# Optimization experiments

Measured on AMD Instinct MI355X. Metric: run time of the kernel, lower is better.

Reference implementation:

```python
import jax, jax.numpy as jnp
import numpy as np

N_HEADS = 8
FACTOR = 5


def layer_norm(x, g, b, eps=1e-5):
    m = x.mean(-1, keepdims=True)
    v = ((x - m) ** 2).mean(-1, keepdims=True)
    return (x - m) / jnp.sqrt(v + eps) * g + b


def prob_attn(q, k, v, factor, key):
    # q,k,v: [B,H,L,E]; mask_flag=False path of ProbAttention
    B, H, L, E = q.shape
    U = min(int(factor * np.ceil(np.log(L))), L)  # sample_k == n_top (L_Q == L_K)
    idx = jax.random.randint(key, (L, U), 0, L)   # random KV sample per query pos
    k_samp = k[:, :, idx, :]                      # gather: [B,H,L,U,E]
    qk_samp = jnp.einsum('bhle,bhlue->bhlu', q, k_samp)
    M = qk_samp.max(-1) - qk_samp.sum(-1) / L     # sparsity measure [B,H,L]
    _, top = jax.lax.top_k(M, U)                  # top-u query indices [B,H,U]
    q_red = jnp.take_along_axis(q, top[..., None], axis=2)  # [B,H,U,E]
    scores = jnp.einsum('bhue,bhke->bhuk', q_red, k) * (1.0 / np.sqrt(E))
    attn = jax.nn.softmax(scores, axis=-1)
    upd = jnp.einsum('bhuk,bhkd->bhud', attn, v)  # [B,H,U,D]
    ctx = jnp.broadcast_to(v.mean(axis=2, keepdims=True), (B, H, L, v.shape[-1]))
    bi = jnp.arange(B)[:, None, None]
    hi = jnp.arange(H)[None, :, None]
    return ctx.at[bi, hi, top].set(upd)          # scatter reduced context


def informer_fwd(x_enc, x_mark_enc, conv_w, Wq, bq, Wk, bk, Wv, bv, Wo, bo,
                 W1, b1, W2, b2, g1, be1, g2, be2, gF, bF, fc_w, fc_b):
    B, L, C = x_enc.shape
    D = conv_w.shape[0]
    H = N_HEADS
    dh = D // H
    # TokenEmbedding: circular Conv1d k=3, no bias
    xp = jnp.transpose(x_enc, (0, 2, 1))                      # [B,C,L]
    xp = jnp.concatenate([xp[..., -1:], xp, xp[..., :1]], axis=-1)
    tok = jax.lax.conv_general_dilated(xp, conv_w, (1,), 'VALID',
                                       dimension_numbers=('NCH', 'OIH', 'NCH'))
    tok = jnp.transpose(tok, (0, 2, 1))                       # [B,L,D]
    # PositionalEmbedding (sinusoid)
    pos = jnp.arange(L, dtype=jnp.float32)[:, None]
    div = jnp.exp(jnp.arange(0, D, 2, dtype=jnp.float32) * (-np.log(10000.0) / D))
    pe = jnp.zeros((L, D), jnp.float32)
    pe = pe.at[:, 0::2].set(jnp.sin(pos * div)).at[:, 1::2].set(jnp.cos(pos * div))
    x = tok + pe
    n_layers = Wq.shape[0]
    for l in range(n_layers):
        q = (x @ Wq[l].T + bq[l]).reshape(B, L, H, dh).transpose(0, 2, 1, 3)
        k = (x @ Wk[l].T + bk[l]).reshape(B, L, H, dh).transpose(0, 2, 1, 3)
        v = (x @ Wv[l].T + bv[l]).reshape(B, L, H, dh).transpose(0, 2, 1, 3)
        ctx = prob_attn(q, k, v, FACTOR, jax.random.fold_in(jax.random.key(42), l))
        # NOTE: original code does .view(B, L, -1) on [B,H,L,dh] WITHOUT transposing
        out = ctx.reshape(B, L, H * dh)
        x = x + (out @ Wo[l].T + bo[l])
        x = layer_norm(x, g1[l], be1[l])
        y = jax.nn.relu(x @ W1[l].T + b1[l]) @ W2[l].T + b2[l]   # 1x1 convs == dense
        x = layer_norm(x + y, g2[l], be2[l])
    x = layer_norm(x, gF, bF)
    out = x * x_mark_enc[..., None]
    out = out.reshape(B, -1)
    return out @ fc_w.T + fc_b


def setup_inputs() -> dict:
    B, L, C, D, H, Dff, EL, NC = 8, 1024, 32, 512, 8, 2048, 3, 16
    key = jax.random.key(0)
    ks = jax.random.split(key, 16)
    rn = lambda k, s, sc=0.02: sc * jax.random.normal(k, s, dtype=jnp.float32)
    return {
        'x_enc': jax.random.normal(ks[0], (B, L, C), dtype=jnp.float32),
        'x_mark_enc': jax.random.uniform(ks[1], (B, L), dtype=jnp.float32),
        'conv_w': rn(ks[2], (D, C, 3), 0.1),
        'Wq': rn(ks[3], (EL, D, D)), 'bq': jnp.zeros((EL, D)),
        'Wk': rn(ks[4], (EL, D, D)), 'bk': jnp.zeros((EL, D)),
        'Wv': rn(ks[5], (EL, D, D)), 'bv': jnp.zeros((EL, D)),
        'Wo': rn(ks[6], (EL, D, D)), 'bo': jnp.zeros((EL, D)),
        'W1': rn(ks[7], (EL, Dff, D)), 'b1': jnp.zeros((EL, Dff)),
        'W2': rn(ks[8], (EL, D, Dff)), 'b2': jnp.zeros((EL, D)),
        'g1': jnp.ones((EL, D)), 'be1': jnp.zeros((EL, D)),
        'g2': jnp.ones((EL, D)), 'be2': jnp.zeros((EL, D)),
        'gF': jnp.ones((D,)), 'bF': jnp.zeros((D,)),
        'fc_w': rn(ks[9], (NC, L * D)), 'fc_b': jnp.zeros((NC,)),
    }


def reference(x_enc, x_mark_enc, conv_w, Wq, bq, Wk, bk, Wv, bv, Wo, bo,
              W1, b1, W2, b2, g1, be1, g2, be2, gF, bF, fc_w, fc_b):
    return informer_fwd(x_enc, x_mark_enc, conv_w, Wq, bq, Wk, bk, Wv, bv, Wo, bo,
                        W1, b1, W2, b2, g1, be1, g2, be2, gF, bF, fc_w, fc_b)
```

## Files before the change

kernel.cpp:

```cpp
#include <hip/hip_runtime.h>
#include <stdint.h>
#include <math.h>

#define LSEQ   1024
#define DMODEL 512
#define NH     8
#define DH     64
#define DFF    2048
#define NB     8
#define NLAYER 3
#define UTOP   35
#define NCLS   16
#define WPERL  3145728

typedef unsigned short u16;
typedef _Float16 f16x8 __attribute__((ext_vector_type(8)));
typedef __attribute__((ext_vector_type(4))) float f32x4;

__device__ __forceinline__ u16 f2h(float f) {
  _Float16 h = (_Float16)f;
  return __builtin_bit_cast(u16, h);
}
__device__ __forceinline__ float h2f(u16 b) {
  return (float)__builtin_bit_cast(_Float16, b);
}

#define GLDS16(gsrc, ldst)                                                        \
  __builtin_amdgcn_global_load_lds(                                              \
      (const __attribute__((address_space(1))) void*)(gsrc),                     \
      (__attribute__((address_space(3))) void*)(ldst), 16, 0, 0)

__host__ __device__ __forceinline__ uint32_t rotl32(uint32_t x, int d) {
  return (x << d) | (x >> (32 - d));
}
__host__ __device__ inline void tf2x32(uint32_t k0, uint32_t k1,
                                       uint32_t c0, uint32_t c1,
                                       uint32_t& o0, uint32_t& o1) {
  uint32_t ks2 = k0 ^ k1 ^ 0x1BD11BDAu;
  uint32_t x0 = c0 + k0, x1 = c1 + k1;
#define TF_R4(a,b,c,d) \
  x0 += x1; x1 = rotl32(x1,(a)); x1 ^= x0; \
  x0 += x1; x1 = rotl32(x1,(b)); x1 ^= x0; \
  x0 += x1; x1 = rotl32(x1,(c)); x1 ^= x0; \
  x0 += x1; x1 = rotl32(x1,(d)); x1 ^= x0;
  TF_R4(13,15,26,6)   x0 += k1;  x1 += ks2 + 1u;
  TF_R4(17,29,16,24)  x0 += ks2; x1 += k0 + 2u;
  TF_R4(13,15,26,6)   x0 += k0;  x1 += k1 + 3u;
  TF_R4(17,29,16,24)  x0 += k1;  x1 += ks2 + 4u;
  TF_R4(13,15,26,6)   x0 += ks2; x1 += k0 + 5u;
#undef TF_R4
  o0 = x0; o1 = x1;
}

__global__ void __launch_bounds__(256) gen_idx_kernel(uint32_t k0, uint32_t k1,
                                                      int* idx) {
  int i = blockIdx.x * 256 + threadIdx.x;
  if (i >= LSEQ * UTOP) return;
  uint32_t a, b;
  tf2x32(k0, k1, 0u, (uint32_t)i, a, b);
  idx[i] = (int)((a ^ b) & (LSEQ - 1));
}

__global__ void __launch_bounds__(256) cvt_all(
    const float* __restrict__ Wq, const float* __restrict__ Wk,
    const float* __restrict__ Wv, const float* __restrict__ Wo,
    const float* __restrict__ W1, const float* __restrict__ W2,
    u16* __restrict__ dst) {
  const size_t total = (size_t)NLAYER * WPERL;
  for (size_t i4 = ((size_t)blockIdx.x * 256 + threadIdx.x) * 4;
       i4 < total; i4 += (size_t)gridDim.x * 256 * 4) {
    int l = (int)(i4 / WPERL);
    int off = (int)(i4 % WPERL);
    const float* src; size_t so;
    if (off < 262144)       { src = Wq; so = (size_t)l * 262144  + off; }
    else if (off < 524288)  { src = Wk; so = (size_t)l * 262144  + off - 262144; }
    else if (off < 786432)  { src = Wv; so = (size_t)l * 262144  + off - 524288; }
    else if (off < 1048576) { src = Wo; so = (size_t)l * 262144  + off - 786432; }
    else if (off < 2097152) { src = W1; so = (size_t)l * 1048576 + off - 1048576; }
    else                    { src = W2; so = (size_t)l * 1048576 + off - 2097152; }
    float4 v = *(const float4*)&src[so];
    ushort4 h;
    h.x = f2h(v.x); h.y = f2h(v.y); h.z = f2h(v.z); h.w = f2h(v.w);
    *(ushort4*)&dst[i4] = h;
  }
}

__global__ void __launch_bounds__(256) conv_pe(const float* __restrict__ xe,
                                               const float* __restrict__ w,
                                               float* __restrict__ xout,
                                               u16* __restrict__ xh) {
  const int d0 = blockIdx.x * 64;
  const int l0 = blockIdx.y * 32;
  const int b  = blockIdx.z;
  const int tid = threadIdx.x;
  const int dl = tid & 63;
  const int lq = tid >> 6;
  __shared__ float ws_[64][97];
  __shared__ float xs[32][37];

  for (int i = tid; i < 64 * 96; i += 256) {
    int dd = i / 96, cc = i - dd * 96;
    ws_[dd][cc] = w[(size_t)(d0 + dd) * 96 + cc];
  }
  for (int i = tid; i < 34 * 32; i += 256) {
    int r = i >> 5, c = i & 31;
    int row = (l0 - 1 + r + LSEQ) & (LSEQ - 1);
    xs[c][r] = xe[((size_t)b * LSEQ + row) * 32 + c];
  }

  const int d = d0 + dl;
  float div = expf((float)(d & ~1) * (-9.210340371976184f / 512.0f));
  float pe[8];
  #pragma unroll
  for (int j = 0; j < 8; ++j) {
    float arg = (float)(l0 + lq * 8 + j) * div;
    pe[j] = (d & 1) ? cosf(arg) : sinf(arg);
  }
  __syncthreads();

  float acc[8] = {};
  #pragma unroll 4
  for (int c = 0; c < 32; ++c) {
    float w0 = ws_[dl][c * 3 + 0];
    float w1 = ws_[dl][c * 3 + 1];
    float w2 = ws_[dl][c * 3 + 2];
    float xv[10];
    #pragma unroll
    for (int r = 0; r < 10; ++r) xv[r] = xs[c][lq * 8 + r];
    #pragma unroll
    for (int j = 0; j < 8; ++j)
      acc[j] += xv[j] * w0 + xv[j + 1] * w1 + xv[j + 2] * w2;
  }
  #pragma unroll
  for (int j = 0; j < 8; ++j) {
    int l = l0 + lq * 8 + j;
    float v = acc[j] + pe[j];
    size_t m = (size_t)b * LSEQ + l;
    xout[m * DMODEL + d] = v;
    xh[m * DMODEL + d] = f2h(v);
  }
}

__global__ void __launch_bounds__(512, 2) gemm256(
    const u16* __restrict__ A, const u16* __restrict__ W,
    const float* __restrict__ bias, const float* __restrict__ bias_k,
    const float* __restrict__ bias_v,
    float* __restrict__ Cf, u16* __restrict__ C2,
    int Kseg, int N, int mode) {
  __shared__ u16 As[2][256 * 64];
  __shared__ u16 Bs[2][256 * 64];
  const int tid = threadIdx.x;
  const int lane = tid & 63, wv = tid >> 6;
  const int wm = wv >> 2, wn = wv & 3;
  const int pid = blockIdx.y * gridDim.x + blockIdx.x;
  const int cpx = (gridDim.x * gridDim.y) >> 3;
  const int swz = (pid & 7) * cpx + (pid >> 3);
  const int m0 = (swz / gridDim.x) * 256, n0 = (swz % gridDim.x) * 256;
  const int lrow = lane >> 3;
  const int kgS = (lane & 7) ^ lrow;
  const int nt = Kseg >> 6;

  f32x4 acc[8][4];
  #pragma unroll
  for (int i = 0; i < 8; ++i)
    #pragma unroll
    for (int j = 0; j < 4; ++j) acc[i][j] = (f32x4){0.f, 0.f, 0.f, 0.f};

  auto STAGE = [&](int kv, int buf) {
    #pragma unroll
    for (int r = 0; r < 4; ++r) {
      int seg = wv * 4 + r;
      int row = seg * 8 + lrow;
      GLDS16(A + (size_t)(m0 + row) * Kseg + kv + kgS * 8, &As[buf][seg * 512]);
      GLDS16(W + (size_t)(n0 + row) * Kseg + kv + kgS * 8, &Bs[buf][seg * 512]);
    }
  };

  STAGE(0, 0);
  for (int t = 0; t < nt; ++t) {
    const int cur = t & 1;
    if (t + 1 < nt) {
      STAGE((t + 1) * 64, cur ^ 1);
      asm volatile("s_waitcnt vmcnt(8)" ::: "memory");
    } else {
      asm volatile("s_waitcnt vmcnt(0)" ::: "memory");
    }
    __builtin_amdgcn_s_barrier();
    __builtin_amdgcn_sched_barrier(0);
    #pragma unroll
    for (int kk = 0; kk < 2; ++kk) {
      int kg = kk * 4 + (lane >> 4);
      f16x8 af[8], bf[4];
      #pragma unroll
      for (int mi = 0; mi < 8; ++mi) {
        int row = wm * 128 + mi * 16 + (lane & 15);
        af[mi] = *(const f16x8*)&As[cur][row * 64 + ((kg ^ (row & 7)) << 3)];
      }
      #pragma unroll
      for (int ni = 0; ni < 4; ++ni) {
        int row = wn * 64 + ni * 16 + (lane & 15);
        bf[ni] = *(const f16x8*)&Bs[cur][row * 64 + ((kg ^ (row & 7)) << 3)];
      }
      #pragma unroll
      for (int mi = 0; mi < 8; ++mi)
        #pragma unroll
        for (int ni = 0; ni < 4; ++ni)
          acc[mi][ni] = __builtin_amdgcn_mfma_f32_16x16x32_f16(
              af[mi], bf[ni], acc[mi][ni], 0, 0, 0);
    }
    __builtin_amdgcn_s_barrier();
  }

  const int colb = n0 + wn * 64 + (lane & 15);
  const int rowb = m0 + wm * 128 + ((lane >> 4) << 2);
  #pragma unroll
  for (int mi = 0; mi < 8; ++mi) {
    #pragma unroll
    for (int ni = 0; ni < 4; ++ni) {
      int gcol = colb + ni * 16;
      float bv;
      if (mode == 3) {
        int mat = gcol >> 9, c = gcol & 511;
        bv = (mat == 0 ? bias : (mat == 1 ? bias_k : bias_v))[c];
      } else {
        bv = bias[gcol];
      }
      #pragma unroll
      for (int j = 0; j < 4; ++j) {
        int grow = rowb + mi * 16 + j;
        float v = acc[mi][ni][j] + bv;
        if (mode == 1) {
          C2[(size_t)grow * N + gcol] = f2h(fmaxf(v, 0.f));
        } else {
          int mat = gcol >> 9, c = gcol & 511;
          Cf[(size_t)mat * (NB * LSEQ * DMODEL) +
             (size_t)(grow >> 10) * (NH * LSEQ * DH) +
             (size_t)(c >> 6) * (LSEQ * DH) +
             (size_t)(grow & (LSEQ - 1)) * DH + (c & (DH - 1))] = v;
        }
      }
    }
  }
}

__global__ void __launch_bounds__(256) gemm_cat(
    const u16* __restrict__ A, const u16* __restrict__ W,
    const float* __restrict__ bias, const float* __restrict__ resid,
    float* __restrict__ Cf, float* __restrict__ Cf1,
    int Kseg, int kslice, int N) {
  __shared__ u16 As[2][128 * 64];
  __shared__ u16 Bs[2][128 * 64];
  const int tid = threadIdx.x;
  const int lane = tid & 63, wv = tid >> 6;
  const int wm = wv >> 1, wn = wv & 1;
  const int pid = blockIdx.y * gridDim.x + blockIdx.x;
  const int cpx = (gridDim.x * gridDim.y) >> 3;
  const int swz = (pid & 7) * cpx + (pid >> 3);
  const int m0 = (swz / gridDim.x) * 128, n0 = (swz % gridDim.x) * 128;
  const int lrow = lane >> 3;
  const int kgS = (lane & 7) ^ lrow;
  const int kv0 = blockIdx.z * kslice;
  const int nt = kslice >> 6;

  f32x4 acc[4][4];
  #pragma unroll
  for (int i = 0; i < 4; ++i)
    #pragma unroll
    for (int j = 0; j < 4; ++j) acc[i][j] = (f32x4){0.f, 0.f, 0.f, 0.f};

  auto STAGE = [&](int kv, int buf) {
    #pragma unroll
    for (int r = 0; r < 4; ++r) {
      int seg = wv * 4 + r;
      int row = seg * 8 + lrow;
      GLDS16(A + (size_t)(m0 + row) * Kseg + kv + kgS * 8, &As[buf][seg * 512]);
      GLDS16(W + (size_t)(n0 + row) * Kseg + kv + kgS * 8, &Bs[buf][seg * 512]);
    }
  };

  STAGE(kv0, 0);
  for (int t = 0; t < nt; ++t) {
    const int cur = t & 1;
    if (t + 1 < nt) {
      STAGE(kv0 + (t + 1) * 64, cur ^ 1);
      asm volatile("s_waitcnt vmcnt(8)" ::: "memory");
    } else {
      asm volatile("s_waitcnt vmcnt(0)" ::: "memory");
    }
    __builtin_amdgcn_s_barrier();
    __builtin_amdgcn_sched_barrier(0);
    #pragma unroll
    for (int kk = 0; kk < 2; ++kk) {
      int kg = kk * 4 + (lane >> 4);
      f16x8 af[4], bf[4];
      #pragma unroll
      for (int mi = 0; mi < 4; ++mi) {
        int row = wm * 64 + mi * 16 + (lane & 15);
        af[mi] = *(const f16x8*)&As[cur][row * 64 + ((kg ^ (row & 7)) << 3)];
      }
      #pragma unroll
      for (int ni = 0; ni < 4; ++ni) {
        int row = wn * 64 + ni * 16 + (lane & 15);
        bf[ni] = *(const f16x8*)&Bs[cur][row * 64 + ((kg ^ (row & 7)) << 3)];
      }
      #pragma unroll
      for (int mi = 0; mi < 4; ++mi)
        #pragma unroll
        for (int ni = 0; ni < 4; ++ni)
          acc[mi][ni] = __builtin_amdgcn_mfma_f32_16x16x32_f16(
              af[mi], bf[ni], acc[mi][ni], 0, 0, 0);
    }
    __builtin_amdgcn_s_barrier();
  }

  const int colb = n0 + wn * 64 + (lane & 15);
  const int rowb = m0 + wm * 64 + ((lane >> 4) << 2);
  const bool z0 = (blockIdx.z == 0);
  float* co = z0 ? Cf : Cf1;
  #pragma unroll
  for (int mi = 0; mi < 4; ++mi) {
    #pragma unroll
    for (int ni = 0; ni < 4; ++ni) {
      int gcol = colb + ni * 16;
      float bv = z0 ? bias[gcol] : 0.f;
      #pragma unroll
      for (int j = 0; j < 4; ++j) {
        int grow = rowb + mi * 16 + j;
        float v = acc[mi][ni][j] + bv;
        size_t o = (size_t)grow * N + gcol;
        if (z0 && resid) v += resid[o];
        co[o] = v;
      }
    }
  }
}

__global__ void __launch_bounds__(256) sampled_m(const float* __restrict__ q,
                                                 const float* __restrict__ k,
                                                 const int* __restrict__ idx,
                                                 float* __restrict__ M) {
  const int g = threadIdx.x >> 6, t = threadIdx.x & 63;
  const int bid = blockIdx.x;
  const int c6 = bid & 63;
  const int bh = ((c6 & 7) << 3) | (c6 >> 3);
  const int l = (bid >> 6) * 4 + g;
  const int bhl = (bh << 10) | l;
  const float4 qv = *(const float4*)&q[(size_t)bhl * DH + (t & 15) * 4];
  const float* kbase = k + (((size_t)bh) << 10) * DH;
  const int* ip = idx + l * UTOP;
  float vmax = -INFINITY, vsum = 0.f;
  #pragma unroll
  for (int b = 0; b < 9; ++b) {
    int u = b * 4 + (t >> 4);
    bool valid = (u < UTOP);
    int kr = valid ? ip[u] : 0;
    float4 kv = *(const float4*)&kbase[(size_t)kr * DH + (t & 15) * 4];
    float p = qv.x * kv.x + qv.y * kv.y + qv.z * kv.z + qv.w * kv.w;
    p += __shfl_xor(p, 1);
    p += __shfl_xor(p, 2);
    p += __shfl_xor(p, 4);
    p += __shfl_xor(p, 8);
    if (valid) { vmax = fmaxf(vmax, p); vsum += p; }
  }
  vmax = fmaxf(vmax, __shfl_down(vmax, 32));
  vmax = fmaxf(vmax, __shfl_down(vmax, 16));
  vsum += __shfl_down(vsum, 32);
  vsum += __shfl_down(vsum, 16);
  if (t == 0) M[bhl] = vmax - vsum * (1.0f / (float)LSEQ);
}

__global__ void __launch_bounds__(256) topk35(const float* __restrict__ M,
                                              int* __restrict__ top) {
  int bh = blockIdx.x;
  int t = threadIdx.x;
  __shared__ float mv[LSEQ];
  __shared__ float rv[256];
  __shared__ int   ri[256];
  for (int i = t; i < LSEQ; i += 256) mv[i] = M[(size_t)bh * LSEQ + i];
  __syncthreads();
  for (int it = 0; it < UTOP; ++it) {
    float bestv = -INFINITY; int besti = 0x7fffffff;
    for (int i = t; i < LSEQ; i += 256) {
      float v = mv[i];
      if (v > bestv || (v == bestv && i < besti)) { bestv = v; besti = i; }
    }
    rv[t] = bestv; ri[t] = besti;
    __syncthreads();
    for (int s = 128; s; s >>= 1) {
      if (t < s) {
        float v2 = rv[t + s]; int i2 = ri[t + s];
        if (v2 > rv[t] || (v2 == rv[t] && i2 < ri[t])) { rv[t] = v2; ri[t] = i2; }
      }
      __syncthreads();
    }
    if (t == 0) { top[bh * UTOP + it] = ri[0]; mv[ri[0]] = -INFINITY; }
    __syncthreads();
  }
}

__global__ void __launch_bounds__(256) vmean_k(const float* __restrict__ v,
                                               float* __restrict__ vm) {
  int bh = blockIdx.x, t = threadIdx.x;
  int e = t & 63, c = t >> 6;
  float s = 0.f;
  for (int l = c * 256; l < (c + 1) * 256; ++l)
    s += v[((size_t)bh * LSEQ + l) * DH + e];
  __shared__ float pr[4][64];
  pr[c][e] = s; __syncthreads();
  if (t < 64)
    vm[bh * DH + t] = (pr[0][t] + pr[1][t] + pr[2][t] + pr[3][t]) * (1.0f / (float)LSEQ);
}

__global__ void __launch_bounds__(256) ctx_fillb(const float* __restrict__ vm,
                                                 u16* __restrict__ ctxh) {
  int j4 = (blockIdx.x * 256 + threadIdx.x) * 4;
  int bh = j4 >> 16;
  int e = j4 & 63;
  float4 v = *(const float4*)&vm[bh * DH + e];
  ushort4 h;
  h.x = f2h(v.x); h.y = f2h(v.y); h.z = f2h(v.z); h.w = f2h(v.w);
  *(ushort4*)&ctxh[(size_t)(j4 >> 9) * 512 + (j4 & 511)] = h;
}

__global__ void __launch_bounds__(512) attn_rows(const float* __restrict__ q,
                                                 const float* __restrict__ k,
                                                 const float* __restrict__ v,
                                                 const int* __restrict__ top,
                                                 u16* __restrict__ ctxh) {
  const int bid = blockIdx.x;
  const int c6 = bid & 63, uc = bid >> 6;
  const int bh = ((c6 & 7) << 3) | (c6 >> 3);
  const int t = threadIdx.x;
  const int lane = t & 63, wvi = t >> 6;
  __shared__ float qs[5][DH];
  __shared__ float sc[5][LSEQ];
  __shared__ float red[5][8];
  __shared__ float part[8][5][DH];
  __shared__ float mxs[5], invs[5];
  int rows[5];
  #pragma unroll
  for (int i = 0; i < 5; ++i) rows[i] = top[bh * UTOP + uc * 5 + i];
  for (int i = t; i < 5 * DH; i += 512) {
    int u = i >> 6, e = i & 63;
    qs[u][e] = q[((size_t)bh * LSEQ + rows[u]) * DH + e];
  }
  __syncthreads();

  float mloc[5] = {-INFINITY, -INFINITY, -INFINITY, -INFINITY, -INFINITY};
  #pragma unroll
  for (int it = 0; it < 2; ++it) {
    int kk = t + it * 512;
    const float4* kp = (const float4*)&k[((size_t)bh * LSEQ + kk) * DH];
    float d[5] = {};
    #pragma unroll
    for (int c0 = 0; c0 < 16; c0 += 8) {
      float4 kr[8];
      #pragma unroll
      for (int e = 0; e < 8; ++e) kr[e] = kp[c0 + e];
      #pragma unroll
      for (int u = 0; u < 5; ++u) {
        const float4* q4 = (const float4*)qs[u];
        #pragma unroll
        for (int e = 0; e < 8; ++e) {
          float4 qv = q4[c0 + e];
          d[u] += qv.x * kr[e].x + qv.y * kr[e].y + qv.z * kr[e].z + qv.w * kr[e].w;
        }
      }
    }
    #pragma unroll
    for (int u = 0; u < 5; ++u) {
      float dv = d[u] * 0.125f;
      sc[u][kk] = dv;
      mloc[u] = fmaxf(mloc[u], dv);
    }
  }
  #pragma unroll
  for (int u = 0; u < 5; ++u) {
    float m = mloc[u];
    #pragma unroll
    for (int off = 32; off; off >>= 1) m = fmaxf(m, __shfl_down(m, off));
    if (lane == 0) red[u][wvi] = m;
  }
  __syncthreads();
  if (t < 5) {
    float m = red[t][0];
    #pragma unroll
    for (int i = 1; i < 8; ++i) m = fmaxf(m, red[t][i]);
    mxs[t] = m;
  }
  __syncthreads();

  float sloc[5] = {};
  #pragma unroll
  for (int it = 0; it < 2; ++it) {
    int kk = t + it * 512;
    #pragma unroll
    for (int u = 0; u < 5; ++u) {
      float p = expf(sc[u][kk] - mxs[u]);
      sc[u][kk] = p;
      sloc[u] += p;
    }
  }
  #pragma unroll
  for (int u = 0; u < 5; ++u) {
    float s = sloc[u];
    #pragma unroll
    for (int off = 32; off; off >>= 1) s += __shfl_down(s, off);
    if (lane == 0) red[u][wvi] = s;
  }
  __syncthreads();
  if (t < 5) {
    float s = 0.f;
    #pragma unroll
    for (int i = 0; i < 8; ++i) s += red[t][i];
    invs[t] = 1.0f / s;
  }
  __syncthreads();

  int e = t & 63, cq = t >> 6;
  float acc[5] = {};
  for (int kk = cq * 128; kk < (cq + 1) * 128; ++kk) {
    float vv = v[((size_t)bh * LSEQ + kk) * DH + e];
    #pragma unroll
    for (int u = 0; u < 5; ++u) acc[u] += sc[u][kk] * vv;
  }
  #pragma unroll
  for (int u = 0; u < 5; ++u) part[cq][u][e] = acc[u];
  __syncthreads();
  for (int i = t; i < 5 * DH; i += 512) {
    int u = i >> 6, ee = i & 63;
    float s = 0.f;
    #pragma unroll
    for (int c = 0; c < 8; ++c) s += part[c][u][ee];
    s *= invs[u];
    size_t lin = ((size_t)bh * LSEQ + rows[u]) * DH + ee;
    ctxh[(lin >> 9) * 512 + (lin & 511)] = f2h(s);
  }
}

__global__ void __launch_bounds__(256) ln_k(const float* __restrict__ in,
                                            const float* __restrict__ in2,
                                            const float* __restrict__ g,
                                            const float* __restrict__ be,
                                            float* __restrict__ out,
                                            u16* __restrict__ oh,
                                            const float* __restrict__ mark) {
  int row = blockIdx.x, t = threadIdx.x;
  size_t o0 = (size_t)row * DMODEL + t, o1 = o0 + 256;
  float x0 = in[o0], x1 = in[o1];
  if (in2) { x0 += in2[o0]; x1 += in2[o1]; }
  __shared__ float red[256];
  red[t] = x0 + x1; __syncthreads();
  for (int s = 128; s; s >>= 1) { if (t < s) red[t] += red[t + s]; __syncthreads(); }
  float mean = red[0] * (1.0f / DMODEL);
  __syncthreads();
  float d0 = x0 - mean, d1 = x1 - mean;
  red[t] = d0 * d0 + d1 * d1; __syncthreads();
  for (int s = 128; s; s >>= 1) { if (t < s) red[t] += red[t + s]; __syncthreads(); }
  float rstd = 1.0f / sqrtf(red[0] * (1.0f / DMODEL) + 1e-5f);
  float v0 = d0 * rstd * g[t] + be[t];
  float v1 = d1 * rstd * g[t + 256] + be[t + 256];
  if (mark) { float mk = mark[row]; v0 *= mk; v1 *= mk; }
  if (out) { out[o0] = v0; out[o1] = v1; }
  if (oh) {
    oh[o0] = f2h(v0);
    oh[o1] = f2h(v1);
  }
}

__global__ void __launch_bounds__(256) fc_stage1(const float* __restrict__ y,
                                                 const float* __restrict__ fw,
                                                 float* __restrict__ part) {
  int blk = blockIdx.x;
  int k0 = blk * 1024;
  int tid = threadIdx.x;
  __shared__ float ys[NB][1024];
  #pragma unroll
  for (int b = 0; b < NB; ++b)
    *(float4*)&ys[b][tid * 4] = *(const float4*)&y[(size_t)b * (LSEQ * DMODEL) + k0 + tid * 4];
  __syncthreads();
  int c = tid & 15, ks = tid >> 4;
  float acc[NB] = {};
  const float* wp = fw + (size_t)c * (LSEQ * DMODEL) + k0 + ks * 64;
  for (int j = 0; j < 16; ++j) {
    int jj = (j + ks) & 15;
    float4 w4 = *(const float4*)&wp[jj * 4];
    #pragma unroll
    for (int b = 0; b < NB; ++b) {
      float4 yv = *(const float4*)&ys[b][ks * 64 + jj * 4];
      acc[b] += yv.x * w4.x + yv.y * w4.y + yv.z * w4.z + yv.w * w4.w;
    }
  }
  __shared__ float rs[16][128];
  #pragma unroll
  for (int b = 0; b < NB; ++b) rs[ks][b * 16 + c] = acc[b];
  __syncthreads();
  if (tid < 128) {
    float s = 0.f;
    #pragma unroll
    for (int i = 0; i < 16; ++i) s += rs[i][tid];
    part[(size_t)tid * 512 + blk] = s;
  }
}

__global__ void __launch_bounds__(128) fc_stage2(const float* __restrict__ part,
                                                 const float* __restrict__ fb,
                                                 float* __restrict__ out) {
  int bc = threadIdx.x;
  float s = 0.f;
  for (int i = 0; i < 512; ++i) s += part[(size_t)bc * 512 + i];
  out[bc] = s + fb[bc & 15];
}

extern "C" void kernel_launch(void* const* d_in, const int* in_sizes, int n_in,
                              void* d_out, int out_size, void* d_ws, size_t ws_size,
                              hipStream_t stream) {
  (void)in_sizes; (void)n_in; (void)out_size; (void)ws_size;
  const float* x_enc  = (const float*)d_in[0];
  const float* x_mark = (const float*)d_in[1];
  const float* conv_w = (const float*)d_in[2];
  const float* Wq = (const float*)d_in[3];
  const float* bq = (const float*)d_in[4];
  const float* Wk = (const float*)d_in[5];
  const float* bk = (const float*)d_in[6];
  const float* Wv = (const float*)d_in[7];
  const float* bv = (const float*)d_in[8];
  const float* Wo = (const float*)d_in[9];
  const float* bo = (const float*)d_in[10];
  const float* W1 = (const float*)d_in[11];
  const float* b1 = (const float*)d_in[12];
  const float* W2 = (const float*)d_in[13];
  const float* b2 = (const float*)d_in[14];
  const float* g1 = (const float*)d_in[15];
  const float* be1= (const float*)d_in[16];
  const float* g2 = (const float*)d_in[17];
  const float* be2= (const float*)d_in[18];
  const float* gF = (const float*)d_in[19];
  const float* bF = (const float*)d_in[20];
  const float* fcw= (const float*)d_in[21];
  const float* fcb= (const float*)d_in[22];
  float* out = (float*)d_out;

  const size_t NBLD = (size_t)NB * LSEQ * DMODEL;
  float* ws   = (float*)d_ws;
  float* xb   = ws;
  float* pre0 = xb   + NBLD;
  float* qb   = pre0 + NBLD;
  float* kb   = qb   + NBLD;
  float* vb   = kb   + NBLD;
  u16*  xh    = (u16*)(vb + NBLD);
  u16*  ctxh  = xh + NBLD;
  u16*  Wcat  = ctxh + NBLD;
  float* Mb   = (float*)(Wcat + (size_t)NLAYER * WPERL);
  float* vm   = Mb + (size_t)NB * NH * LSEQ;
  float* part = vm + NB * NH * DH;
  int* idxb   = (int*)(part + 512 * 128);
  int* topb   = idxb + LSEQ * UTOP;
  u16* hidh   = (u16*)qb;
  float* preB = qb;
  float* preC = vb;

  cvt_all<<<2048, 256, 0, stream>>>(Wq, Wk, Wv, Wo, W1, W2, Wcat);

  {
    dim3 gc(8, 32, NB);
    conv_pe<<<gc, 256, 0, stream>>>(x_enc, conv_w, xb, xh);
  }

  dim3 gqkv(6,  32);
  dim3 gw1 (8,  32);
  dim3 gwo (4,  64, 2);
  dim3 gw2 (4,  64, 2);

  for (int l = 0; l < NLAYER; ++l) {
    const u16* Wl    = Wcat + (size_t)l * WPERL;
    const u16* Wc_qkv= Wl;
    const u16* Wc_o  = Wl + 786432;
    const u16* Wc_1  = Wl + 1048576;
    const u16* Wc_2  = Wl + 2097152;

    gemm256<<<gqkv, 512, 0, stream>>>(xh, Wc_qkv,
                                      bq + l*DMODEL, bk + l*DMODEL, bv + l*DMODEL,
                                      qb, nullptr, 512, 1536, 3);

    uint32_t lk0, lk1, k2_0, k2_1;
    tf2x32(0u, 42u, 0u, (uint32_t)l, lk0, lk1);
    tf2x32(lk0, lk1, 0u, 1u, k2_0, k2_1);
    gen_idx_kernel<<<140, 256, 0, stream>>>(k2_0, k2_1, idxb);
    sampled_m<<<NB * NH * LSEQ / 4, 256, 0, stream>>>(qb, kb, idxb, Mb);
    topk35<<<NB * NH, 256, 0, stream>>>(Mb, topb);
    vmean_k<<<NB * NH, 256, 0, stream>>>(vb, vm);
    ctx_fillb<<<(NB * NH * LSEQ * DH) / 1024, 256, 0, stream>>>(vm, ctxh);
    attn_rows<<<448, 512, 0, stream>>>(qb, kb, vb, topb, ctxh);

    gemm_cat<<<gwo, 256, 0, stream>>>(ctxh, Wc_o, bo + l*DMODEL,
                                      xb, pre0, preB, 512, 256, 512);
    ln_k<<<NB * LSEQ, 256, 0, stream>>>(pre0, preB, g1 + l*DMODEL, be1 + l*DMODEL,
                                        xb, xh, nullptr);

    gemm256<<<gw1, 512, 0, stream>>>(xh, Wc_1,
                                     b1 + l*DFF, nullptr, nullptr,
                                     nullptr, hidh, 512, 2048, 1);
    gemm_cat<<<gw2, 256, 0, stream>>>(hidh, Wc_2, b2 + l*DMODEL,
                                      xb, pre0, preC, 2048, 1024, 512);
    ln_k<<<NB * LSEQ, 256, 0, stream>>>(pre0, preC, g2 + l*DMODEL, be2 + l*DMODEL,
                                        xb, xh, nullptr);
  }

  ln_k<<<NB * LSEQ, 256, 0, stream>>>(xb, nullptr, gF, bF, pre0, nullptr, x_mark);
  fc_stage1<<<512, 256, 0, stream>>>(pre0, fcw, part);
  fc_stage2<<<1, 128, 0, stream>>>(part, fcb, out);
}
```

Measured before the change: 998.3 us.

## Split reduced attention over key quarters with a flash-style merge kernel

The single attn_rows kernel (448 blocks of 512 threads, each covering all 1024 keys) is replaced by attn_part, which splits the keys into four quarters across 1792 blocks of 256 threads. Each block writes its partial max, partial sum and unnormalised output. A new attn_merge kernel then combines the partials with log-sum-exp rescaling and writes the fp16 context rows. The aim is more parallelism and occupancy on the GPU for this small attention stage, at the cost of one extra launch and a round trip of partial results through global memory.

```diff
diff --git a/kernel.cpp b/kernel.cpp
--- a/kernel.cpp
+++ b/kernel.cpp
@@ -422,118 +422,133 @@
   *(ushort4*)&ctxh[(size_t)(j4 >> 9) * 512 + (j4 & 511)] = h;
 }
 
-__global__ void __launch_bounds__(512) attn_rows(const float* __restrict__ q,
+__global__ void __launch_bounds__(256) attn_part(const float* __restrict__ q,
                                                  const float* __restrict__ k,
                                                  const float* __restrict__ v,
                                                  const int* __restrict__ top,
-                                                 u16* __restrict__ ctxh) {
+                                                 float* __restrict__ pm,
+                                                 float* __restrict__ ps,
+                                                 float* __restrict__ po) {
+  const int bid = blockIdx.x;
+  const int c6 = bid & 63;
+  const int bh = ((c6 & 7) << 3) | (c6 >> 3);
+  const int rest = bid >> 6;
+  const int uc = rest >> 2, qtr = rest & 3;
+  const int k0 = qtr * 256;
+  const int t = threadIdx.x;
+  const int lane = t & 63, wvi = t >> 6;
+  __shared__ float qs[5][DH];
+  __shared__ float sc[5][256];
+  __shared__ float red[5][4];
+  __shared__ float part[4][5][DH];
+  __shared__ float mxs[5];
+  int rows[5];
+  #pragma unroll
+  for (int i = 0; i < 5; ++i) rows[i] = top[bh * UTOP + uc * 5 + i];
+  for (int i = t; i < 5 * DH; i += 256) {
+    int u = i >> 6, e = i & 63;
+    qs[u][e] = q[((size_t)bh * LSEQ + rows[u]) * DH + e];
+  }
+  __syncthreads();
+
+  const float4* kp = (const float4*)&k[((size_t)bh * LSEQ + k0 + t) * DH];
+  float d[5] = {};
+  #pragma unroll
+  for (int c0 = 0; c0 < 16; c0 += 8) {
+    float4 kr[8];
+    #pragma unroll
+    for (int e = 0; e < 8; ++e) kr[e] = kp[c0 + e];
+    #pragma unroll
+    for (int u = 0; u < 5; ++u) {
+      const float4* q4 = (const float4*)qs[u];
+      #pragma unroll
+      for (int e = 0; e < 8; ++e) {
+        float4 qv = q4[c0 + e];
+        d[u] += qv.x * kr[e].x + qv.y * kr[e].y + qv.z * kr[e].z + qv.w * kr[e].w;
+      }
+    }
+  }
+  #pragma unroll
+  for (int u = 0; u < 5; ++u) {
+    float dv = d[u] * 0.125f;
+    sc[u][t] = dv;
+    float m = dv;
+    #pragma unroll
+    for (int off = 32; off; off >>= 1) m = fmaxf(m, __shfl_down(m, off));
+    if (lane == 0) red[u][wvi] = m;
+  }
+  __syncthreads();
+  if (t < 5)
+    mxs[t] = fmaxf(fmaxf(red[t][0], red[t][1]), fmaxf(red[t][2], red[t][3]));
+  __syncthreads();
+
+  #pragma unroll
+  for (int u = 0; u < 5; ++u) {
+    float p = expf(sc[u][t] - mxs[u]);
+    sc[u][t] = p;
+    #pragma unroll
+    for (int off = 32; off; off >>= 1) p += __shfl_down(p, off);
+    if (lane == 0) red[u][wvi] = p;
+  }
+  __syncthreads();
+
+  int e = t & 63, cq = t >> 6;
+  float acc[5] = {};
+  for (int kk = cq * 64; kk < (cq + 1) * 64; ++kk) {
+    float vv = v[((size_t)bh * LSEQ + k0 + kk) * DH + e];
+    #pragma unroll
+    for (int u = 0; u < 5; ++u) acc[u] += sc[u][kk] * vv;
+  }
+  #pragma unroll
+  for (int u = 0; u < 5; ++u) part[cq][u][e] = acc[u];
+  __syncthreads();
+
+  const int slot = (bh * 7 + uc) * 4 + qtr;
+  if (t < 5) {
+    pm[slot * 5 + t] = mxs[t];
+    ps[slot * 5 + t] = red[t][0] + red[t][1] + red[t][2] + red[t][3];
+  }
+  for (int i = t; i < 5 * DH; i += 256) {
+    int u = i >> 6, ee = i & 63;
+    po[((size_t)slot * 5 + u) * 64 + ee] =
+        part[0][u][ee] + part[1][u][ee] + part[2][u][ee] + part[3][u][ee];
+  }
+}
+
+__global__ void __launch_bounds__(256) attn_merge(const float* __restrict__ pm,
+                                                  const float* __restrict__ ps,
+                                                  const float* __restrict__ po,
+                                                  const int* __restrict__ top,
+                                                  u16* __restrict__ ctxh) {
   const int bid = blockIdx.x;
   const int c6 = bid & 63, uc = bid >> 6;
   const int bh = ((c6 & 7) << 3) | (c6 >> 3);
   const int t = threadIdx.x;
-  const int lane = t & 63, wvi = t >> 6;
-  __shared__ float qs[5][DH];
-  __shared__ float sc[5][LSEQ];
-  __shared__ float red[5][8];
-  __shared__ float part[8][5][DH];
-  __shared__ float mxs[5], invs[5];
-  int rows[5];
-  #pragma unroll
-  for (int i = 0; i < 5; ++i) rows[i] = top[bh * UTOP + uc * 5 + i];
-  for (int i = t; i < 5 * DH; i += 512) {
+  const int base = (bh * 7 + uc) * 4;
+  __shared__ float wgt[5][4];
+  __shared__ float inv[5];
+  __shared__ int rows[5];
+  if (t < 5) {
+    rows[t] = top[bh * UTOP + uc * 5 + t];
+    float m0 = pm[(base + 0) * 5 + t], m1 = pm[(base + 1) * 5 + t];
+    float m2 = pm[(base + 2) * 5 + t], m3 = pm[(base + 3) * 5 + t];
+    float M = fmaxf(fmaxf(m0, m1), fmaxf(m2, m3));
+    float w0 = expf(m0 - M), w1 = expf(m1 - M);
+    float w2 = expf(m2 - M), w3 = expf(m3 - M);
+    float S = ps[(base + 0) * 5 + t] * w0 + ps[(base + 1) * 5 + t] * w1 +
+              ps[(base + 2) * 5 + t] * w2 + ps[(base + 3) * 5 + t] * w3;
+    wgt[t][0] = w0; wgt[t][1] = w1; wgt[t][2] = w2; wgt[t][3] = w3;
+    inv[t] = 1.0f / S;
+  }
+  __syncthreads();
+  for (int i = t; i < 5 * DH; i += 256) {
     int u = i >> 6, e = i & 63;
-    qs[u][e] = q[((size_t)bh * LSEQ + rows[u]) * DH + e];
-  }
-  __syncthreads();
-
-  float mloc[5] = {-INFINITY, -INFINITY, -INFINITY, -INFINITY, -INFINITY};
-  #pragma unroll
-  for (int it = 0; it < 2; ++it) {
-    int kk = t + it * 512;
-    const float4* kp = (const float4*)&k[((size_t)bh * LSEQ + kk) * DH];
-    float d[5] = {};
-    #pragma unroll
-    for (int c0 = 0; c0 < 16; c0 += 8) {
-      float4 kr[8];
-      #pragma unroll
-      for (int e = 0; e < 8; ++e) kr[e] = kp[c0 + e];
-      #pragma unroll
-      for (int u = 0; u < 5; ++u) {
-        const float4* q4 = (const float4*)qs[u];
-        #pragma unroll
-        for (int e = 0; e < 8; ++e) {
-          float4 qv = q4[c0 + e];
-          d[u] += qv.x * kr[e].x + qv.y * kr[e].y + qv.z * kr[e].z + qv.w * kr[e].w;
-        }
-      }
-    }
-    #pragma unroll
-    for (int u = 0; u < 5; ++u) {
-      float dv = d[u] * 0.125f;
-      sc[u][kk] = dv;
-      mloc[u] = fmaxf(mloc[u], dv);
-    }
-  }
-  #pragma unroll
-  for (int u = 0; u < 5; ++u) {
-    float m = mloc[u];
-    #pragma unroll
-    for (int off = 32; off; off >>= 1) m = fmaxf(m, __shfl_down(m, off));
-    if (lane == 0) red[u][wvi] = m;
-  }
-  __syncthreads();
-  if (t < 5) {
-    float m = red[t][0];
-    #pragma unroll
-    for (int i = 1; i < 8; ++i) m = fmaxf(m, red[t][i]);
-    mxs[t] = m;
-  }
-  __syncthreads();
-
-  float sloc[5] = {};
-  #pragma unroll
-  for (int it = 0; it < 2; ++it) {
-    int kk = t + it * 512;
-    #pragma unroll
-    for (int u = 0; u < 5; ++u) {
-      float p = expf(sc[u][kk] - mxs[u]);
-      sc[u][kk] = p;
-      sloc[u] += p;
-    }
-  }
-  #pragma unroll
-  for (int u = 0; u < 5; ++u) {
-    float s = sloc[u];
-    #pragma unroll
-    for (int off = 32; off; off >>= 1) s += __shfl_down(s, off);
-    if (lane == 0) red[u][wvi] = s;
-  }
-  __syncthreads();
-  if (t < 5) {
-    float s = 0.f;
-    #pragma unroll
-    for (int i = 0; i < 8; ++i) s += red[t][i];
-    invs[t] = 1.0f / s;
-  }
-  __syncthreads();
-
-  int e = t & 63, cq = t >> 6;
-  float acc[5] = {};
-  for (int kk = cq * 128; kk < (cq + 1) * 128; ++kk) {
-    float vv = v[((size_t)bh * LSEQ + kk) * DH + e];
-    #pragma unroll
-    for (int u = 0; u < 5; ++u) acc[u] += sc[u][kk] * vv;
-  }
-  #pragma unroll
-  for (int u = 0; u < 5; ++u) part[cq][u][e] = acc[u];
-  __syncthreads();
-  for (int i = t; i < 5 * DH; i += 512) {
-    int u = i >> 6, ee = i & 63;
-    float s = 0.f;
-    #pragma unroll
-    for (int c = 0; c < 8; ++c) s += part[c][u][ee];
-    s *= invs[u];
-    size_t lin = ((size_t)bh * LSEQ + rows[u]) * DH + ee;
+    float o = po[((size_t)(base + 0) * 5 + u) * 64 + e] * wgt[u][0] +
+              po[((size_t)(base + 1) * 5 + u) * 64 + e] * wgt[u][1] +
+              po[((size_t)(base + 2) * 5 + u) * 64 + e] * wgt[u][2] +
+              po[((size_t)(base + 3) * 5 + u) * 64 + e] * wgt[u][3];
+    float s = o * inv[u];
+    size_t lin = ((size_t)bh * LSEQ + rows[u]) * DH + e;
     ctxh[(lin >> 9) * 512 + (lin & 511)] = f2h(s);
   }
 }
@@ -656,6 +671,9 @@
   float* part = vm + NB * NH * DH;
   int* idxb   = (int*)(part + 512 * 128);
   int* topb   = idxb + LSEQ * UTOP;
+  float* pmb  = (float*)(topb + NB * NH * UTOP);
+  float* psb  = pmb + 1792 * 5;
+  float* pob  = psb + 1792 * 5;
   u16* hidh   = (u16*)qb;
   float* preB = qb;
   float* preC = vb;
@@ -691,7 +709,8 @@
     topk35<<<NB * NH, 256, 0, stream>>>(Mb, topb);
     vmean_k<<<NB * NH, 256, 0, stream>>>(vb, vm);
     ctx_fillb<<<(NB * NH * LSEQ * DH) / 1024, 256, 0, stream>>>(vm, ctxh);
-    attn_rows<<<448, 512, 0, stream>>>(qb, kb, vb, topb, ctxh);
+    attn_part<<<1792, 256, 0, stream>>>(qb, kb, vb, topb, pmb, psb, pob);
+    attn_merge<<<448, 256, 0, stream>>>(pmb, psb, pob, topb, ctxh);
 
     gemm_cat<<<gwo, 256, 0, stream>>>(ctxh, Wc_o, bo + l*DMODEL,
                                       xb, pre0, preB, 512, 256, 512);
```

Result: no change. 1.017 ms (+1.9%).
